# Performance work log

Hardware: AMD Instinct MI355X
Metric: run time of the kernel (lower is better)

The kernel has to match this reference:

```python
import jax, jax.numpy as jnp
import numpy as np

B, C, E, H = 2, 2048, 1024, 16
HD = E // H


def setup_inputs() -> dict:
    key = jax.random.key(0)
    k_x, k_len, k_w1, k_b1, k_w2, k_b2 = jax.random.split(key, 6)
    x = jax.random.normal(k_x, (B, C, E), dtype=jnp.float32)
    # pad_mask: True where token is valid; random valid lengths in [C//2, C]
    lengths = jax.random.randint(k_len, (B,), C // 2, C + 1)
    pad_mask = jnp.arange(C)[None, :] < lengths[:, None]  # [B, C] bool
    s1 = 1.0 / np.sqrt(E)
    w_qkv = jax.random.uniform(k_w1, (3 * E, E), jnp.float32, -s1, s1)  # torch Linear weight [out,in]
    b_qkv = jax.random.uniform(k_b1, (3 * E,), jnp.float32, -s1, s1)
    w_out = jax.random.uniform(k_w2, (E, E), jnp.float32, -s1, s1)
    b_out = jax.random.uniform(k_b2, (E,), jnp.float32, -s1, s1)
    return {"x": x, "pad_mask": pad_mask, "w_qkv": w_qkv, "b_qkv": b_qkv,
            "w_out": w_out, "b_out": b_out}


def reference(x, pad_mask, w_qkv, b_qkv, w_out, b_out):
    b, c, e = x.shape
    qkv = x @ w_qkv.T + b_qkv                      # [B, C, 3E]
    qkv = qkv.reshape(b, c, 3, H, HD)
    qkv = jnp.transpose(qkv, (2, 0, 3, 1, 4))      # [3, B, H, C, HD]
    q, k, v = qkv[0], qkv[1], qkv[2]
    scores = jnp.einsum('bhqd,bhkd->bhqk', q, k) / np.sqrt(HD)  # [B,H,C,C]
    causal = jnp.tril(jnp.ones((c, c), dtype=bool))
    scores = jnp.where(causal[None, None, :, :], scores, -1e9)
    scores = jnp.where(pad_mask[:, None, None, :], scores, -1e9)
    attn = jax.nn.softmax(scores, axis=-1)
    out = jnp.einsum('bhqk,bhkd->bhqd', attn, v)   # [B,H,C,HD]
    out = jnp.transpose(out, (0, 2, 1, 3)).reshape(b, c, e)
    return out @ w_out.T + b_out
```

## Files before the change

kernel.cpp:

```cpp
#include <hip/hip_runtime.h>
#include <cstdint>
#include <cstddef>

typedef short short8 __attribute__((ext_vector_type(8)));
typedef float f32x4 __attribute__((ext_vector_type(4)));

#define NB 2
#define NC 2048
#define NE 1024
#define NH 16
#define ND 64
#define QSZ (NB*NH*NC*ND)

typedef const __attribute__((address_space(1))) void GV;
typedef __attribute__((address_space(3))) void LV;

__device__ __forceinline__ unsigned short f32_to_bf16(float f) {
    union { float f; unsigned u; } v; v.f = f;
    return (unsigned short)((v.u + 0x7fffu + ((v.u >> 16) & 1u)) >> 16);
}

__global__ __launch_bounds__(256) void fused_cast_kernel(
    const float* __restrict__ x, const float* __restrict__ wqkv,
    const float* __restrict__ wout, const void* __restrict__ pad,
    unsigned short* __restrict__ x_bf, unsigned short* __restrict__ wqkv_bf,
    unsigned short* __restrict__ wout_bf, int* __restrict__ lengths)
{
    const int bid = blockIdx.x, tid = threadIdx.x;
    if (bid < 8192) {
        const float* src; unsigned short* dst; int i;
        if (bid < 4096)      { src = x;    dst = x_bf;    i = bid*256 + tid; }
        else if (bid < 7168) { src = wqkv; dst = wqkv_bf; i = (bid-4096)*256 + tid; }
        else                 { src = wout; dst = wout_bf; i = (bid-7168)*256 + tid; }
        float4 v = ((const float4*)src)[i];
        ushort4 o;
        o.x = f32_to_bf16(v.x); o.y = f32_to_bf16(v.y);
        o.z = f32_to_bf16(v.z); o.w = f32_to_bf16(v.w);
        ((ushort4*)dst)[i] = o;
    } else {
        const int b = bid - 8192;
        unsigned w0 = ((const unsigned*)pad)[0];
        int cnt = 0;
        for (int i = tid; i < NC; i += 256) {
            int idx = b*NC + i;
            bool valid;
            if (w0 == 1u)               valid = ((const int*)pad)[idx] != 0;
            else if (w0 == 0x3f800000u) valid = ((const float*)pad)[idx] != 0.0f;
            else                        valid = ((const unsigned char*)pad)[idx] != 0;
            cnt += valid ? 1 : 0;
        }
        cnt += __shfl_xor(cnt, 1);  cnt += __shfl_xor(cnt, 2);
        cnt += __shfl_xor(cnt, 4);  cnt += __shfl_xor(cnt, 8);
        cnt += __shfl_xor(cnt, 16); cnt += __shfl_xor(cnt, 32);
        __shared__ int ws_[4];
        if ((tid & 63) == 0) ws_[tid >> 6] = cnt;
        __syncthreads();
        if (tid == 0) lengths[b] = ws_[0] + ws_[1] + ws_[2] + ws_[3];
    }
}

template<int EPI, int TM, int WPE>
__global__ __launch_bounds__(256, WPE) void gemm_bt_kernel(
    const unsigned short* __restrict__ A,
    const unsigned short* __restrict__ Bw,
    const float* __restrict__ bias,
    const int* __restrict__ lengths,
    float* __restrict__ outF,
    unsigned short* __restrict__ outQ,
    int M, int N, int K)
{
    constexpr int NF = (TM == 128) ? 4 : 2;
    constexpr int WCW = 16 * NF;
    __shared__ unsigned short As[TM*64];
    __shared__ unsigned short Bs[128*64];
    const int tid = threadIdx.x;
    const int w = tid >> 6, lane = tid & 63;
    const int wr = (TM == 128) ? (w >> 1) : 0;
    const int wc = (TM == 128) ? (w & 1) : w;
    const int g = lane >> 4, lr = lane & 15;
    const int nbx = N >> 7, nwg = gridDim.x;
    const int id = blockIdx.x;
    const int swz = (id & 7) * (nwg >> 3) + (id >> 3);
    const int mBase = (swz / nbx) * TM, nBase = (swz % nbx) * 128;

    if constexpr (EPI == 1) {
        if (nBase >= 1024) {
            const int lb = lengths[mBase >> 11];
            if ((mBase & 2047) >= ((lb + 63) & ~63)) return;
        }
    }

    f32x4 acc[4][NF];
#pragma unroll
    for (int m = 0; m < 4; ++m)
#pragma unroll
        for (int n = 0; n < NF; ++n) acc[m][n] = (f32x4){0.f, 0.f, 0.f, 0.f};

    constexpr int AJ = TM / 32;
    int srow[4], scol[4]; unsigned ldso[4];
#pragma unroll
    for (int j = 0; j < 4; ++j) {
        int o = ((j*4 + w) << 10) + lane*16;
        int row = o >> 7;
        int chunk = ((o >> 4) & 7) ^ (row & 7);
        srow[j] = row; scol[j] = chunk * 8; ldso[j] = (unsigned)((j*4 + w) << 10);
    }

    const int nk = K >> 6;
    for (int kt = 0; kt < nk; ++kt) {
        const int k0 = kt << 6;
#pragma unroll
        for (int j = 0; j < AJ; ++j) {
            const unsigned short* ga = A + (size_t)(mBase + srow[j])*K + (k0 + scol[j]);
            __builtin_amdgcn_global_load_lds((GV*)ga, (LV*)((char*)As + ldso[j]), 16, 0, 0);
        }
#pragma unroll
        for (int j = 0; j < 4; ++j) {
            const unsigned short* gb = Bw + (size_t)(nBase + srow[j])*K + (k0 + scol[j]);
            __builtin_amdgcn_global_load_lds((GV*)gb, (LV*)((char*)Bs + ldso[j]), 16, 0, 0);
        }
        __syncthreads();
#pragma unroll
        for (int ks = 0; ks < 2; ++ks) {
            short8 af[4], bf[NF];
#pragma unroll
            for (int m = 0; m < 4; ++m) {
                int row = wr*64 + m*16 + lr;
                int chunk = (ks*4 + g) ^ (row & 7);
                af[m] = *(const short8*)((const char*)As + row*128 + chunk*16);
            }
#pragma unroll
            for (int n = 0; n < NF; ++n) {
                int row = wc*WCW + n*16 + lr;
                int chunk = (ks*4 + g) ^ (row & 7);
                bf[n] = *(const short8*)((const char*)Bs + row*128 + chunk*16);
            }
#pragma unroll
            for (int m = 0; m < 4; ++m)
#pragma unroll
                for (int n = 0; n < NF; ++n)
                    acc[m][n] = __builtin_amdgcn_mfma_f32_16x16x32_bf16(af[m], bf[n], acc[m][n], 0, 0, 0);
        }
        __syncthreads();
    }

    if constexpr (EPI == 0) {
#pragma unroll
        for (int n = 0; n < NF; ++n) {
            int col = nBase + wc*WCW + n*16 + lr;
            float bv = bias[col];
#pragma unroll
            for (int m = 0; m < 4; ++m) {
                int rowb = mBase + wr*64 + m*16 + 4*g;
#pragma unroll
                for (int r = 0; r < 4; ++r)
                    outF[(size_t)(rowb + r)*N + col] = acc[m][n][r] + bv;
            }
        }
    } else {
        if (nBase >= 2048) {
#pragma unroll
            for (int n = 0; n < NF; ++n) {
                int col = nBase + wc*WCW + n*16 + lr;
                float bv = bias[col];
                int hh = (col >> 6) & 15, d = col & 63;
#pragma unroll
                for (int m = 0; m < 4; ++m) {
                    int rowb = mBase + wr*64 + m*16 + 4*g;
                    int bb = rowb >> 11, c = rowb & 2047;
                    int cp = (c & ~63) | ((m >> 1) << 5) | (g << 3) | ((m & 1) << 2);
                    size_t base = (((size_t)((4 + bb)*16 + hh))*64 + d)*2048 + cp;
                    float v0 = acc[m][n][0] + bv, v1 = acc[m][n][1] + bv;
                    float v2 = acc[m][n][2] + bv, v3 = acc[m][n][3] + bv;
                    unsigned w0, w1;
                    asm("v_cvt_pk_bf16_f32 %0, %1, %2" : "=v"(w0) : "v"(v0), "v"(v1));
                    asm("v_cvt_pk_bf16_f32 %0, %1, %2" : "=v"(w1) : "v"(v2), "v"(v3));
                    union { unsigned u[2]; uint2 v; } pk2; pk2.u[0] = w0; pk2.u[1] = w1;
                    *(uint2*)(outQ + base) = pk2.v;
                }
            }
        } else {
#pragma unroll
            for (int n = 0; n < NF; ++n) {
                int col = nBase + wc*WCW + n*16 + lr;
                float bv = bias[col];
                int t = col >> 10, hh = (col >> 6) & 15, d = col & 63;
                float qscale = (t == 0) ? 0.1803368801f : 1.0f;
#pragma unroll
                for (int m = 0; m < 4; ++m) {
                    int rowb = mBase + wr*64 + m*16 + 4*g;
#pragma unroll
                    for (int r = 0; r < 4; ++r) {
                        int row = rowb + r;
                        int bb = row >> 11, c = row & 2047;
                        unsigned short bf16v = f32_to_bf16((acc[m][n][r] + bv) * qscale);
                        size_t idx = ((((size_t)(t*2 + bb))*16 + hh)*2048 + c)*64 + d;
                        outQ[idx] = bf16v;
                    }
                }
            }
        }
    }
}

__global__ __launch_bounds__(256, 4) void attn_kernel(
    const unsigned short* __restrict__ qkv,
    const int* __restrict__ lengths,
    unsigned short* __restrict__ ctx)
{
    __shared__ unsigned short KVt[4][64*64];
    const int bh = blockIdx.x;
    const int b = bh >> 4, h = bh & 15;
    const int y = blockIdx.y;
    const int qb = (y < 8) ? 31 - y : (y < 16) ? y - 8 : (y < 24) ? 39 - y : y - 16;
    const int q0 = qb * 64;
    const int len = lengths[b];
    const int nt = min(qb + 1, (len + 63) >> 6);
    const int tid = threadIdx.x, w = tid >> 6, lane = tid & 63;
    const int g = lane >> 4, lr = lane & 15;
    const unsigned short* qp = qkv +          ((size_t)(b*NH + h))*NC*ND;
    const unsigned short* kp = qkv + QSZ    + ((size_t)(b*NH + h))*NC*ND;
    const unsigned short* vp = qkv + 2*QSZ  + ((size_t)(b*NH + h))*ND*NC;
    const int qw0 = q0 + w*16;

    short8 aq[2];
#pragma unroll
    for (int ks = 0; ks < 2; ++ks)
        aq[ks] = *(const short8*)(qp + (size_t)(qw0 + lr)*ND + ks*32 + 8*g);

    f32x4 oa[4];
#pragma unroll
    for (int n = 0; n < 4; ++n) oa[n] = (f32x4){0.f, 0.f, 0.f, 0.f};
    f32x4 acc_l = (f32x4){0.f, 0.f, 0.f, 0.f};
    union { unsigned u[4]; short8 s; } ones;
    ones.u[0] = ones.u[1] = ones.u[2] = ones.u[3] = 0x3F803F80u;

    const char* kv0 = (char*)KVt + lr*128 + (((g    ) ^ (lr & 7)) << 4);
    const char* kv1 = (char*)KVt + lr*128 + (((4 + g) ^ (lr & 7)) << 4);

    int srw0, sck0, srw1, sck1; unsigned ldso0, ldso1;
    {
        int o0 = (w << 10) + lane*16;
        int r0 = o0 >> 7;
        sck0 = (((o0 >> 4) & 7) ^ (r0 & 7)) * 8; srw0 = r0;
        ldso0 = (unsigned)(w << 10);
        int o1 = ((4 + w) << 10) + lane*16;
        int r1 = o1 >> 7;
        sck1 = (((o1 >> 4) & 7) ^ (r1 & 7)) * 8; srw1 = r1;
        ldso1 = (unsigned)((4 + w) << 10);
    }
    const unsigned short* gk0 = kp + (size_t)srw0*ND + sck0;
    const unsigned short* gk1 = kp + (size_t)srw1*ND + sck1;
    const unsigned short* gv0 = vp + (size_t)srw0*NC + sck0;
    const unsigned short* gv1 = vp + (size_t)srw1*NC + sck1;

#define STAGE(BUF) do {                                                           \
    __builtin_amdgcn_global_load_lds((GV*)gk0, (LV*)((char*)KVt + (BUF)*8192 + ldso0), 16, 0, 0);          \
    __builtin_amdgcn_global_load_lds((GV*)gv0, (LV*)((char*)KVt + 16384 + (BUF)*8192 + ldso0), 16, 0, 0);  \
    __builtin_amdgcn_global_load_lds((GV*)gk1, (LV*)((char*)KVt + (BUF)*8192 + ldso1), 16, 0, 0);          \
    __builtin_amdgcn_global_load_lds((GV*)gv1, (LV*)((char*)KVt + 16384 + (BUF)*8192 + ldso1), 16, 0, 0);  \
    gk0 += 64*ND; gk1 += 64*ND; gv0 += 64; gv1 += 64; } while (0)

    STAGE(0);
    __syncthreads();

#pragma unroll 2
    for (int t = 0; t < nt - 1; ++t) {
        STAGE((t + 1) & 1);
        const int buf = t & 1;

        f32x4 sa[4];
#pragma unroll
        for (int a = 0; a < 4; ++a) sa[a] = (f32x4){0.f, 0.f, 0.f, 0.f};
        __builtin_amdgcn_s_setprio(1);
#pragma unroll
        for (int a = 0; a < 4; ++a) {
            short8 ak = *(const short8*)(kv0 + buf*8192 + a*2048);
            sa[a] = __builtin_amdgcn_mfma_f32_16x16x32_bf16(ak, aq[0], sa[a], 0, 0, 0);
        }
#pragma unroll
        for (int a = 0; a < 4; ++a) {
            short8 ak = *(const short8*)(kv1 + buf*8192 + a*2048);
            sa[a] = __builtin_amdgcn_mfma_f32_16x16x32_bf16(ak, aq[1], sa[a], 0, 0, 0);
        }
        __builtin_amdgcn_s_setprio(0);

        float p[4][4];
#pragma unroll
        for (int a = 0; a < 4; ++a)
#pragma unroll
            for (int r = 0; r < 4; ++r)
                p[a][r] = __builtin_amdgcn_exp2f(sa[a][r]);

        unsigned pw0, pw1, pw2, pw3, pw4, pw5, pw6, pw7;
        asm("v_cvt_pk_bf16_f32 %0, %1, %2" : "=v"(pw0) : "v"(p[0][0]), "v"(p[0][1]));
        asm("v_cvt_pk_bf16_f32 %0, %1, %2" : "=v"(pw1) : "v"(p[0][2]), "v"(p[0][3]));
        asm("v_cvt_pk_bf16_f32 %0, %1, %2" : "=v"(pw2) : "v"(p[1][0]), "v"(p[1][1]));
        asm("v_cvt_pk_bf16_f32 %0, %1, %2" : "=v"(pw3) : "v"(p[1][2]), "v"(p[1][3]));
        asm("v_cvt_pk_bf16_f32 %0, %1, %2" : "=v"(pw4) : "v"(p[2][0]), "v"(p[2][1]));
        asm("v_cvt_pk_bf16_f32 %0, %1, %2" : "=v"(pw5) : "v"(p[2][2]), "v"(p[2][3]));
        asm("v_cvt_pk_bf16_f32 %0, %1, %2" : "=v"(pw6) : "v"(p[3][0]), "v"(p[3][1]));
        asm("v_cvt_pk_bf16_f32 %0, %1, %2" : "=v"(pw7) : "v"(p[3][2]), "v"(p[3][3]));
        union { unsigned u[4]; short8 s; } pu0, pu1;
        pu0.u[0] = pw0; pu0.u[1] = pw1; pu0.u[2] = pw2; pu0.u[3] = pw3;
        pu1.u[0] = pw4; pu1.u[1] = pw5; pu1.u[2] = pw6; pu1.u[3] = pw7;

        __builtin_amdgcn_s_setprio(1);
        acc_l = __builtin_amdgcn_mfma_f32_16x16x32_bf16(pu0.s, ones.s, acc_l, 0, 0, 0);
#pragma unroll
        for (int n = 0; n < 4; ++n) {
            short8 bv = *(const short8*)(kv0 + 16384 + buf*8192 + n*2048);
            oa[n] = __builtin_amdgcn_mfma_f32_16x16x32_bf16(pu0.s, bv, oa[n], 0, 0, 0);
        }
        acc_l = __builtin_amdgcn_mfma_f32_16x16x32_bf16(pu1.s, ones.s, acc_l, 0, 0, 0);
#pragma unroll
        for (int n = 0; n < 4; ++n) {
            short8 bv = *(const short8*)(kv1 + 16384 + buf*8192 + n*2048);
            oa[n] = __builtin_amdgcn_mfma_f32_16x16x32_bf16(pu1.s, bv, oa[n], 0, 0, 0);
        }
        __builtin_amdgcn_s_setprio(0);

        __syncthreads();
    }

    {
        const int t = nt - 1;
        const int boff = (t & 1) * 8192;
        const char* k0b = kv0 + boff;
        const char* k1b = kv1 + boff;
        const int thr = min(qw0 + lr, len - 1);
        const int kb0 = (t << 6) + 4*g;

        f32x4 sa[4];
#pragma unroll
        for (int a = 0; a < 4; ++a) sa[a] = (f32x4){0.f, 0.f, 0.f, 0.f};
        __builtin_amdgcn_s_setprio(1);
#pragma unroll
        for (int a = 0; a < 4; ++a) {
            short8 ak = *(const short8*)(k0b + a*2048);
            sa[a] = __builtin_amdgcn_mfma_f32_16x16x32_bf16(ak, aq[0], sa[a], 0, 0, 0);
        }
#pragma unroll
        for (int a = 0; a < 4; ++a) {
            short8 ak = *(const short8*)(k1b + a*2048);
            sa[a] = __builtin_amdgcn_mfma_f32_16x16x32_bf16(ak, aq[1], sa[a], 0, 0, 0);
        }
        __builtin_amdgcn_s_setprio(0);

        float p[4][4];
#pragma unroll
        for (int a = 0; a < 4; ++a)
#pragma unroll
            for (int r = 0; r < 4; ++r) {
                int key = kb0 + 16*a + r;
                p[a][r] = (key <= thr) ? __builtin_amdgcn_exp2f(sa[a][r]) : 0.f;
            }

        unsigned pw0, pw1, pw2, pw3, pw4, pw5, pw6, pw7;
        asm("v_cvt_pk_bf16_f32 %0, %1, %2" : "=v"(pw0) : "v"(p[0][0]), "v"(p[0][1]));
        asm("v_cvt_pk_bf16_f32 %0, %1, %2" : "=v"(pw1) : "v"(p[0][2]), "v"(p[0][3]));
        asm("v_cvt_pk_bf16_f32 %0, %1, %2" : "=v"(pw2) : "v"(p[1][0]), "v"(p[1][1]));
        asm("v_cvt_pk_bf16_f32 %0, %1, %2" : "=v"(pw3) : "v"(p[1][2]), "v"(p[1][3]));
        asm("v_cvt_pk_bf16_f32 %0, %1, %2" : "=v"(pw4) : "v"(p[2][0]), "v"(p[2][1]));
        asm("v_cvt_pk_bf16_f32 %0, %1, %2" : "=v"(pw5) : "v"(p[2][2]), "v"(p[2][3]));
        asm("v_cvt_pk_bf16_f32 %0, %1, %2" : "=v"(pw6) : "v"(p[3][0]), "v"(p[3][1]));
        asm("v_cvt_pk_bf16_f32 %0, %1, %2" : "=v"(pw7) : "v"(p[3][2]), "v"(p[3][3]));
        union { unsigned u[4]; short8 s; } pu0, pu1;
        pu0.u[0] = pw0; pu0.u[1] = pw1; pu0.u[2] = pw2; pu0.u[3] = pw3;
        pu1.u[0] = pw4; pu1.u[1] = pw5; pu1.u[2] = pw6; pu1.u[3] = pw7;

        __builtin_amdgcn_s_setprio(1);
        acc_l = __builtin_amdgcn_mfma_f32_16x16x32_bf16(pu0.s, ones.s, acc_l, 0, 0, 0);
#pragma unroll
        for (int n = 0; n < 4; ++n) {
            short8 bv = *(const short8*)(k0b + 16384 + n*2048);
            oa[n] = __builtin_amdgcn_mfma_f32_16x16x32_bf16(pu0.s, bv, oa[n], 0, 0, 0);
        }
        acc_l = __builtin_amdgcn_mfma_f32_16x16x32_bf16(pu1.s, ones.s, acc_l, 0, 0, 0);
#pragma unroll
        for (int n = 0; n < 4; ++n) {
            short8 bv = *(const short8*)(k1b + 16384 + n*2048);
            oa[n] = __builtin_amdgcn_mfma_f32_16x16x32_bf16(pu1.s, bv, oa[n], 0, 0, 0);
        }
        __builtin_amdgcn_s_setprio(0);
    }
#undef STAGE

#pragma unroll
    for (int r = 0; r < 4; ++r) {
        float inv = __builtin_amdgcn_rcpf(acc_l[r]);
        int qg = qw0 + 4*g + r;
        size_t base = ((size_t)b*NC + qg)*NE + h*ND;
#pragma unroll
        for (int n = 0; n < 4; ++n)
            ctx[base + n*16 + lr] = f32_to_bf16(oa[n][r] * inv);
    }
}

extern "C" void kernel_launch(void* const* d_in, const int* in_sizes, int n_in,
                              void* d_out, int out_size, void* d_ws, size_t ws_size,
                              hipStream_t stream)
{
    const float* x    = (const float*)d_in[0];
    const void*  pad  = d_in[1];
    const float* wqkv = (const float*)d_in[2];
    const float* bqkv = (const float*)d_in[3];
    const float* wout = (const float*)d_in[4];
    const float* bout = (const float*)d_in[5];
    float* out = (float*)d_out;

    unsigned short* x_bf    = (unsigned short*)d_ws;
    unsigned short* wqkv_bf = x_bf    + 4194304;
    unsigned short* wout_bf = wqkv_bf + 3145728;
    unsigned short* qkv     = wout_bf + 1048576;
    unsigned short* ctx     = qkv     + 12582912;
    int*            lens    = (int*)(ctx + 4194304);

    fused_cast_kernel<<<8194, 256, 0, stream>>>(x, wqkv, wout, pad,
                                                x_bf, wqkv_bf, wout_bf, lens);

    gemm_bt_kernel<1,128,3><<<768, 256, 0, stream>>>(x_bf, wqkv_bf, bqkv, lens,
                                                     nullptr, qkv, 4096, 3072, 1024);
    attn_kernel<<<dim3(32, 32), 256, 0, stream>>>(qkv, lens, ctx);
    gemm_bt_kernel<0,64,2><<<512, 256, 0, stream>>>(ctx, wout_bf, bout, lens,
                                                    out, nullptr, 4096, 1024, 1024);
}
```

Before: 83.65 us.

## Split long causal attention query blocks across two KV halves with merge kernel

Query blocks 16-31 now process their keys in two launches: keys 0-1023 in one block and keys 1024 onward in another. Both write unnormalized partial outputs and row sums in fp32 to workspace, and a new merge kernel adds them, normalizes and writes bf16 context. This splits the long causal rows so the per-block work is more even and more blocks run in parallel. The cost is an extra kernel launch and fp32 partial traffic through global memory. Merging without a running max is safe only because the existing kernel already uses plain exp2 with no max subtraction.

```diff
diff --git a/kernel.cpp b/kernel.cpp
--- a/kernel.cpp
+++ b/kernel.cpp
@@ -206,16 +206,22 @@
 __global__ __launch_bounds__(256, 4) void attn_kernel(
     const unsigned short* __restrict__ qkv,
     const int* __restrict__ lengths,
-    unsigned short* __restrict__ ctx)
+    unsigned short* __restrict__ ctx,
+    float* __restrict__ paO,
+    float* __restrict__ paL)
 {
     __shared__ unsigned short KVt[4][64*64];
     const int bh = blockIdx.x;
     const int b = bh >> 4, h = bh & 15;
     const int y = blockIdx.y;
-    const int qb = (y < 8) ? 31 - y : (y < 16) ? y - 8 : (y < 24) ? 39 - y : y - 16;
+    int qb, c0, mode;
+    if (y < 16)      { mode = 1; qb = 16 + y;        c0 = 0;  }
+    else if (y < 32) { mode = 0; qb = 31 - y;        c0 = 0;  }
+    else             { mode = 2; qb = 16 + (47 - y); c0 = 16; }
     const int q0 = qb * 64;
     const int len = lengths[b];
-    const int nt = min(qb + 1, (len + 63) >> 6);
+    const int lenceil = (len + 63) >> 6;
+    const int c1 = (mode == 1) ? 16 : min(qb + 1, lenceil);
     const int tid = threadIdx.x, w = tid >> 6, lane = tid & 63;
     const int g = lane >> 4, lr = lane & 15;
     const unsigned short* qp = qkv +          ((size_t)(b*NH + h))*NC*ND;
@@ -249,10 +255,10 @@
         sck1 = (((o1 >> 4) & 7) ^ (r1 & 7)) * 8; srw1 = r1;
         ldso1 = (unsigned)((4 + w) << 10);
     }
-    const unsigned short* gk0 = kp + (size_t)srw0*ND + sck0;
-    const unsigned short* gk1 = kp + (size_t)srw1*ND + sck1;
-    const unsigned short* gv0 = vp + (size_t)srw0*NC + sck0;
-    const unsigned short* gv1 = vp + (size_t)srw1*NC + sck1;
+    const unsigned short* gk0 = kp + (size_t)(c0*64 + srw0)*ND + sck0;
+    const unsigned short* gk1 = kp + (size_t)(c0*64 + srw1)*ND + sck1;
+    const unsigned short* gv0 = vp + (size_t)srw0*NC + c0*64 + sck0;
+    const unsigned short* gv1 = vp + (size_t)srw1*NC + c0*64 + sck1;
 
 #define STAGE(BUF) do {                                                           \
     __builtin_amdgcn_global_load_lds((GV*)gk0, (LV*)((char*)KVt + (BUF)*8192 + ldso0), 16, 0, 0);          \
@@ -261,139 +267,178 @@
     __builtin_amdgcn_global_load_lds((GV*)gv1, (LV*)((char*)KVt + 16384 + (BUF)*8192 + ldso1), 16, 0, 0);  \
     gk0 += 64*ND; gk1 += 64*ND; gv0 += 64; gv1 += 64; } while (0)
 
-    STAGE(0);
-    __syncthreads();
-
+    if (!(mode == 2 && c1 <= 16)) {
+        STAGE(0);
+        __syncthreads();
+
+        const int nfast = ((mode == 1) ? c1 : c1 - 1) - c0;
 #pragma unroll 2
-    for (int t = 0; t < nt - 1; ++t) {
-        STAGE((t + 1) & 1);
-        const int buf = t & 1;
-
-        f32x4 sa[4];
-#pragma unroll
-        for (int a = 0; a < 4; ++a) sa[a] = (f32x4){0.f, 0.f, 0.f, 0.f};
-        __builtin_amdgcn_s_setprio(1);
-#pragma unroll
-        for (int a = 0; a < 4; ++a) {
-            short8 ak = *(const short8*)(kv0 + buf*8192 + a*2048);
-            sa[a] = __builtin_amdgcn_mfma_f32_16x16x32_bf16(ak, aq[0], sa[a], 0, 0, 0);
-        }
-#pragma unroll
-        for (int a = 0; a < 4; ++a) {
-            short8 ak = *(const short8*)(kv1 + buf*8192 + a*2048);
-            sa[a] = __builtin_amdgcn_mfma_f32_16x16x32_bf16(ak, aq[1], sa[a], 0, 0, 0);
-        }
-        __builtin_amdgcn_s_setprio(0);
-
-        float p[4][4];
-#pragma unroll
-        for (int a = 0; a < 4; ++a)
-#pragma unroll
-            for (int r = 0; r < 4; ++r)
-                p[a][r] = __builtin_amdgcn_exp2f(sa[a][r]);
-
-        unsigned pw0, pw1, pw2, pw3, pw4, pw5, pw6, pw7;
-        asm("v_cvt_pk_bf16_f32 %0, %1, %2" : "=v"(pw0) : "v"(p[0][0]), "v"(p[0][1]));
-        asm("v_cvt_pk_bf16_f32 %0, %1, %2" : "=v"(pw1) : "v"(p[0][2]), "v"(p[0][3]));
-        asm("v_cvt_pk_bf16_f32 %0, %1, %2" : "=v"(pw2) : "v"(p[1][0]), "v"(p[1][1]));
-        asm("v_cvt_pk_bf16_f32 %0, %1, %2" : "=v"(pw3) : "v"(p[1][2]), "v"(p[1][3]));
-        asm("v_cvt_pk_bf16_f32 %0, %1, %2" : "=v"(pw4) : "v"(p[2][0]), "v"(p[2][1]));
-        asm("v_cvt_pk_bf16_f32 %0, %1, %2" : "=v"(pw5) : "v"(p[2][2]), "v"(p[2][3]));
-        asm("v_cvt_pk_bf16_f32 %0, %1, %2" : "=v"(pw6) : "v"(p[3][0]), "v"(p[3][1]));
-        asm("v_cvt_pk_bf16_f32 %0, %1, %2" : "=v"(pw7) : "v"(p[3][2]), "v"(p[3][3]));
-        union { unsigned u[4]; short8 s; } pu0, pu1;
-        pu0.u[0] = pw0; pu0.u[1] = pw1; pu0.u[2] = pw2; pu0.u[3] = pw3;
-        pu1.u[0] = pw4; pu1.u[1] = pw5; pu1.u[2] = pw6; pu1.u[3] = pw7;
-
-        __builtin_amdgcn_s_setprio(1);
-        acc_l = __builtin_amdgcn_mfma_f32_16x16x32_bf16(pu0.s, ones.s, acc_l, 0, 0, 0);
-#pragma unroll
-        for (int n = 0; n < 4; ++n) {
-            short8 bv = *(const short8*)(kv0 + 16384 + buf*8192 + n*2048);
-            oa[n] = __builtin_amdgcn_mfma_f32_16x16x32_bf16(pu0.s, bv, oa[n], 0, 0, 0);
-        }
-        acc_l = __builtin_amdgcn_mfma_f32_16x16x32_bf16(pu1.s, ones.s, acc_l, 0, 0, 0);
-#pragma unroll
-        for (int n = 0; n < 4; ++n) {
-            short8 bv = *(const short8*)(kv1 + 16384 + buf*8192 + n*2048);
-            oa[n] = __builtin_amdgcn_mfma_f32_16x16x32_bf16(pu1.s, bv, oa[n], 0, 0, 0);
-        }
-        __builtin_amdgcn_s_setprio(0);
-
-        __syncthreads();
-    }
-
-    {
-        const int t = nt - 1;
-        const int boff = (t & 1) * 8192;
-        const char* k0b = kv0 + boff;
-        const char* k1b = kv1 + boff;
-        const int thr = min(qw0 + lr, len - 1);
-        const int kb0 = (t << 6) + 4*g;
-
-        f32x4 sa[4];
-#pragma unroll
-        for (int a = 0; a < 4; ++a) sa[a] = (f32x4){0.f, 0.f, 0.f, 0.f};
-        __builtin_amdgcn_s_setprio(1);
-#pragma unroll
-        for (int a = 0; a < 4; ++a) {
-            short8 ak = *(const short8*)(k0b + a*2048);
-            sa[a] = __builtin_amdgcn_mfma_f32_16x16x32_bf16(ak, aq[0], sa[a], 0, 0, 0);
-        }
-#pragma unroll
-        for (int a = 0; a < 4; ++a) {
-            short8 ak = *(const short8*)(k1b + a*2048);
-            sa[a] = __builtin_amdgcn_mfma_f32_16x16x32_bf16(ak, aq[1], sa[a], 0, 0, 0);
-        }
-        __builtin_amdgcn_s_setprio(0);
-
-        float p[4][4];
-#pragma unroll
-        for (int a = 0; a < 4; ++a)
-#pragma unroll
-            for (int r = 0; r < 4; ++r) {
-                int key = kb0 + 16*a + r;
-                p[a][r] = (key <= thr) ? __builtin_amdgcn_exp2f(sa[a][r]) : 0.f;
-            }
-
-        unsigned pw0, pw1, pw2, pw3, pw4, pw5, pw6, pw7;
-        asm("v_cvt_pk_bf16_f32 %0, %1, %2" : "=v"(pw0) : "v"(p[0][0]), "v"(p[0][1]));
-        asm("v_cvt_pk_bf16_f32 %0, %1, %2" : "=v"(pw1) : "v"(p[0][2]), "v"(p[0][3]));
-        asm("v_cvt_pk_bf16_f32 %0, %1, %2" : "=v"(pw2) : "v"(p[1][0]), "v"(p[1][1]));
-        asm("v_cvt_pk_bf16_f32 %0, %1, %2" : "=v"(pw3) : "v"(p[1][2]), "v"(p[1][3]));
-        asm("v_cvt_pk_bf16_f32 %0, %1, %2" : "=v"(pw4) : "v"(p[2][0]), "v"(p[2][1]));
-        asm("v_cvt_pk_bf16_f32 %0, %1, %2" : "=v"(pw5) : "v"(p[2][2]), "v"(p[2][3]));
-        asm("v_cvt_pk_bf16_f32 %0, %1, %2" : "=v"(pw6) : "v"(p[3][0]), "v"(p[3][1]));
-        asm("v_cvt_pk_bf16_f32 %0, %1, %2" : "=v"(pw7) : "v"(p[3][2]), "v"(p[3][3]));
-        union { unsigned u[4]; short8 s; } pu0, pu1;
-        pu0.u[0] = pw0; pu0.u[1] = pw1; pu0.u[2] = pw2; pu0.u[3] = pw3;
-        pu1.u[0] = pw4; pu1.u[1] = pw5; pu1.u[2] = pw6; pu1.u[3] = pw7;
-
-        __builtin_amdgcn_s_setprio(1);
-        acc_l = __builtin_amdgcn_mfma_f32_16x16x32_bf16(pu0.s, ones.s, acc_l, 0, 0, 0);
-#pragma unroll
-        for (int n = 0; n < 4; ++n) {
-            short8 bv = *(const short8*)(k0b + 16384 + n*2048);
-            oa[n] = __builtin_amdgcn_mfma_f32_16x16x32_bf16(pu0.s, bv, oa[n], 0, 0, 0);
-        }
-        acc_l = __builtin_amdgcn_mfma_f32_16x16x32_bf16(pu1.s, ones.s, acc_l, 0, 0, 0);
-#pragma unroll
-        for (int n = 0; n < 4; ++n) {
-            short8 bv = *(const short8*)(k1b + 16384 + n*2048);
-            oa[n] = __builtin_amdgcn_mfma_f32_16x16x32_bf16(pu1.s, bv, oa[n], 0, 0, 0);
-        }
-        __builtin_amdgcn_s_setprio(0);
+        for (int tt = 0; tt < nfast; ++tt) {
+            STAGE((tt + 1) & 1);
+            const int buf = tt & 1;
+
+            f32x4 sa[4];
+#pragma unroll
+            for (int a = 0; a < 4; ++a) sa[a] = (f32x4){0.f, 0.f, 0.f, 0.f};
+            __builtin_amdgcn_s_setprio(1);
+#pragma unroll
+            for (int a = 0; a < 4; ++a) {
+                short8 ak = *(const short8*)(kv0 + buf*8192 + a*2048);
+                sa[a] = __builtin_amdgcn_mfma_f32_16x16x32_bf16(ak, aq[0], sa[a], 0, 0, 0);
+            }
+#pragma unroll
+            for (int a = 0; a < 4; ++a) {
+                short8 ak = *(const short8*)(kv1 + buf*8192 + a*2048);
+                sa[a] = __builtin_amdgcn_mfma_f32_16x16x32_bf16(ak, aq[1], sa[a], 0, 0, 0);
+            }
+            __builtin_amdgcn_s_setprio(0);
+
+            float p[4][4];
+#pragma unroll
+            for (int a = 0; a < 4; ++a)
+#pragma unroll
+                for (int r = 0; r < 4; ++r)
+                    p[a][r] = __builtin_amdgcn_exp2f(sa[a][r]);
+
+            unsigned pw0, pw1, pw2, pw3, pw4, pw5, pw6, pw7;
+            asm("v_cvt_pk_bf16_f32 %0, %1, %2" : "=v"(pw0) : "v"(p[0][0]), "v"(p[0][1]));
+            asm("v_cvt_pk_bf16_f32 %0, %1, %2" : "=v"(pw1) : "v"(p[0][2]), "v"(p[0][3]));
+            asm("v_cvt_pk_bf16_f32 %0, %1, %2" : "=v"(pw2) : "v"(p[1][0]), "v"(p[1][1]));
+            asm("v_cvt_pk_bf16_f32 %0, %1, %2" : "=v"(pw3) : "v"(p[1][2]), "v"(p[1][3]));
+            asm("v_cvt_pk_bf16_f32 %0, %1, %2" : "=v"(pw4) : "v"(p[2][0]), "v"(p[2][1]));
+            asm("v_cvt_pk_bf16_f32 %0, %1, %2" : "=v"(pw5) : "v"(p[2][2]), "v"(p[2][3]));
+            asm("v_cvt_pk_bf16_f32 %0, %1, %2" : "=v"(pw6) : "v"(p[3][0]), "v"(p[3][1]));
+            asm("v_cvt_pk_bf16_f32 %0, %1, %2" : "=v"(pw7) : "v"(p[3][2]), "v"(p[3][3]));
+            union { unsigned u[4]; short8 s; } pu0, pu1;
+            pu0.u[0] = pw0; pu0.u[1] = pw1; pu0.u[2] = pw2; pu0.u[3] = pw3;
+            pu1.u[0] = pw4; pu1.u[1] = pw5; pu1.u[2] = pw6; pu1.u[3] = pw7;
+
+            __builtin_amdgcn_s_setprio(1);
+            acc_l = __builtin_amdgcn_mfma_f32_16x16x32_bf16(pu0.s, ones.s, acc_l, 0, 0, 0);
+#pragma unroll
+            for (int n = 0; n < 4; ++n) {
+                short8 bv = *(const short8*)(kv0 + 16384 + buf*8192 + n*2048);
+                oa[n] = __builtin_amdgcn_mfma_f32_16x16x32_bf16(pu0.s, bv, oa[n], 0, 0, 0);
+            }
+            acc_l = __builtin_amdgcn_mfma_f32_16x16x32_bf16(pu1.s, ones.s, acc_l, 0, 0, 0);
+#pragma unroll
+            for (int n = 0; n < 4; ++n) {
+                short8 bv = *(const short8*)(kv1 + 16384 + buf*8192 + n*2048);
+                oa[n] = __builtin_amdgcn_mfma_f32_16x16x32_bf16(pu1.s, bv, oa[n], 0, 0, 0);
+            }
+            __builtin_amdgcn_s_setprio(0);
+
+            __syncthreads();
+        }
+
+        if (mode != 1) {
+            const int boff = (nfast & 1) * 8192;
+            const char* k0b = kv0 + boff;
+            const char* k1b = kv1 + boff;
+            const int thr = min(qw0 + lr, len - 1);
+            const int kb0 = ((c1 - 1) << 6) + 4*g;
+
+            f32x4 sa[4];
+#pragma unroll
+            for (int a = 0; a < 4; ++a) sa[a] = (f32x4){0.f, 0.f, 0.f, 0.f};
+            __builtin_amdgcn_s_setprio(1);
+#pragma unroll
+            for (int a = 0; a < 4; ++a) {
+                short8 ak = *(const short8*)(k0b + a*2048);
+                sa[a] = __builtin_amdgcn_mfma_f32_16x16x32_bf16(ak, aq[0], sa[a], 0, 0, 0);
+            }
+#pragma unroll
+            for (int a = 0; a < 4; ++a) {
+                short8 ak = *(const short8*)(k1b + a*2048);
+                sa[a] = __builtin_amdgcn_mfma_f32_16x16x32_bf16(ak, aq[1], sa[a], 0, 0, 0);
+            }
+            __builtin_amdgcn_s_setprio(0);
+
+            float p[4][4];
+#pragma unroll
+            for (int a = 0; a < 4; ++a)
+#pragma unroll
+                for (int r = 0; r < 4; ++r) {
+                    int key = kb0 + 16*a + r;
+                    p[a][r] = (key <= thr) ? __builtin_amdgcn_exp2f(sa[a][r]) : 0.f;
+                }
+
+            unsigned pw0, pw1, pw2, pw3, pw4, pw5, pw6, pw7;
+            asm("v_cvt_pk_bf16_f32 %0, %1, %2" : "=v"(pw0) : "v"(p[0][0]), "v"(p[0][1]));
+            asm("v_cvt_pk_bf16_f32 %0, %1, %2" : "=v"(pw1) : "v"(p[0][2]), "v"(p[0][3]));
+            asm("v_cvt_pk_bf16_f32 %0, %1, %2" : "=v"(pw2) : "v"(p[1][0]), "v"(p[1][1]));
+            asm("v_cvt_pk_bf16_f32 %0, %1, %2" : "=v"(pw3) : "v"(p[1][2]), "v"(p[1][3]));
+            asm("v_cvt_pk_bf16_f32 %0, %1, %2" : "=v"(pw4) : "v"(p[2][0]), "v"(p[2][1]));
+            asm("v_cvt_pk_bf16_f32 %0, %1, %2" : "=v"(pw5) : "v"(p[2][2]), "v"(p[2][3]));
+            asm("v_cvt_pk_bf16_f32 %0, %1, %2" : "=v"(pw6) : "v"(p[3][0]), "v"(p[3][1]));
+            asm("v_cvt_pk_bf16_f32 %0, %1, %2" : "=v"(pw7) : "v"(p[3][2]), "v"(p[3][3]));
+            union { unsigned u[4]; short8 s; } pu0, pu1;
+            pu0.u[0] = pw0; pu0.u[1] = pw1; pu0.u[2] = pw2; pu0.u[3] = pw3;
+            pu1.u[0] = pw4; pu1.u[1] = pw5; pu1.u[2] = pw6; pu1.u[3] = pw7;
+
+            __builtin_amdgcn_s_setprio(1);
+            acc_l = __builtin_amdgcn_mfma_f32_16x16x32_bf16(pu0.s, ones.s, acc_l, 0, 0, 0);
+#pragma unroll
+            for (int n = 0; n < 4; ++n) {
+                short8 bv = *(const short8*)(k0b + 16384 + n*2048);
+                oa[n] = __builtin_amdgcn_mfma_f32_16x16x32_bf16(pu0.s, bv, oa[n], 0, 0, 0);
+            }
+            acc_l = __builtin_amdgcn_mfma_f32_16x16x32_bf16(pu1.s, ones.s, acc_l, 0, 0, 0);
+#pragma unroll
+            for (int n = 0; n < 4; ++n) {
+                short8 bv = *(const short8*)(k1b + 16384 + n*2048);
+                oa[n] = __builtin_amdgcn_mfma_f32_16x16x32_bf16(pu1.s, bv, oa[n], 0, 0, 0);
+            }
+            __builtin_amdgcn_s_setprio(0);
+        }
     }
 #undef STAGE
 
-#pragma unroll
-    for (int r = 0; r < 4; ++r) {
-        float inv = __builtin_amdgcn_rcpf(acc_l[r]);
-        int qg = qw0 + 4*g + r;
-        size_t base = ((size_t)b*NC + qg)*NE + h*ND;
-#pragma unroll
-        for (int n = 0; n < 4; ++n)
-            ctx[base + n*16 + lr] = f32_to_bf16(oa[n][r] * inv);
+    if (mode == 0) {
+#pragma unroll
+        for (int r = 0; r < 4; ++r) {
+            float inv = __builtin_amdgcn_rcpf(acc_l[r]);
+            int qg = qw0 + 4*g + r;
+            size_t base = ((size_t)b*NC + qg)*NE + h*ND;
+#pragma unroll
+            for (int n = 0; n < 4; ++n)
+                ctx[base + n*16 + lr] = f32_to_bf16(oa[n][r] * inv);
+        }
+    } else {
+        const int grp = bh*16 + (qb - 16);
+        float* po = paO + (size_t)(mode - 1)*2097152 + (size_t)grp*4096;
+        float* pl = paL + (mode - 1)*32768 + grp*64;
+#pragma unroll
+        for (int r = 0; r < 4; ++r) {
+            int prow = w*16 + 4*g + r;
+            pl[prow] = acc_l[r];
+#pragma unroll
+            for (int n = 0; n < 4; ++n)
+                po[prow*64 + n*16 + lr] = oa[n][r];
+        }
+    }
+}
+
+__global__ __launch_bounds__(256) void attn_merge_kernel(
+    const float* __restrict__ paO, const float* __restrict__ paL,
+    unsigned short* __restrict__ ctx)
+{
+    const int grp = blockIdx.x;
+    const int bh = grp >> 4, qm = grp & 15;
+    const int b = bh >> 4, h = bh & 15;
+    const int qb = 16 + qm;
+    const float* oA = paO + (size_t)grp*4096;
+    const float* oB = oA + 2097152;
+    const float* lA = paL + grp*64;
+    const float* lB = lA + 32768;
+#pragma unroll
+    for (int i = 0; i < 16; ++i) {
+        int idx = threadIdx.x + i*256;
+        int row = idx >> 6, d = idx & 63;
+        float l = lA[row] + lB[row];
+        float v = (oA[idx] + oB[idx]) * __builtin_amdgcn_rcpf(l);
+        int qg = qb*64 + row;
+        ctx[((size_t)(b*NC + qg))*NE + h*ND + d] = f32_to_bf16(v);
     }
 }
 
@@ -415,13 +460,16 @@
     unsigned short* qkv     = wout_bf + 1048576;
     unsigned short* ctx     = qkv     + 12582912;
     int*            lens    = (int*)(ctx + 4194304);
+    float*          paO     = (float*)((char*)d_ws + 50331712);
+    float*          paL     = paO + 2*2097152;
 
     fused_cast_kernel<<<8194, 256, 0, stream>>>(x, wqkv, wout, pad,
                                                 x_bf, wqkv_bf, wout_bf, lens);
 
     gemm_bt_kernel<1,128,3><<<768, 256, 0, stream>>>(x_bf, wqkv_bf, bqkv, lens,
                                                      nullptr, qkv, 4096, 3072, 1024);
-    attn_kernel<<<dim3(32, 32), 256, 0, stream>>>(qkv, lens, ctx);
+    attn_kernel<<<dim3(32, 48), 256, 0, stream>>>(qkv, lens, ctx, paO, paL);
+    attn_merge_kernel<<<512, 256, 0, stream>>>(paO, paL, ctx);
     gemm_bt_kernel<0,64,2><<<512, 256, 0, stream>>>(ctx, wout_bf, bout, lens,
                                                     out, nullptr, 4096, 1024, 1024);
 }
```

Result: slower. 89.80 us (+7.4%).

## Triple-buffer K/V tiles in attention with one barrier per iteration

Applied to the files above, without the earlier changes.

The attention kernel's shared K/V staging moves from double to triple buffering. Two tiles are prefetched up front. Each iteration waits with a partial `s_waitcnt vmcnt(4)` plus a raw barrier, instead of a full `__syncthreads` at the end of the loop. This keeps two tile loads in flight while the current tile is computed, hiding more global-load latency. In exchange, shared memory rises from 32 KB to 48 KB per block, and launch bounds drop to 3 blocks per CU, which reduces occupancy. The prefetch also reads one tile past the causal range, which may read slightly out of bounds at the end of the buffer.

```diff
diff --git a/kernel.cpp b/kernel.cpp
--- a/kernel.cpp
+++ b/kernel.cpp
@@ -203,12 +203,12 @@
     }
 }
 
-__global__ __launch_bounds__(256, 4) void attn_kernel(
+__global__ __launch_bounds__(256, 3) void attn_kernel(
     const unsigned short* __restrict__ qkv,
     const int* __restrict__ lengths,
     unsigned short* __restrict__ ctx)
 {
-    __shared__ unsigned short KVt[4][64*64];
+    __shared__ unsigned short KVt[6][64*64];
     const int bh = blockIdx.x;
     const int b = bh >> 4, h = bh & 15;
     const int y = blockIdx.y;
@@ -255,19 +255,26 @@
     const unsigned short* gv1 = vp + (size_t)srw1*NC + sck1;
 
 #define STAGE(BUF) do {                                                           \
-    __builtin_amdgcn_global_load_lds((GV*)gk0, (LV*)((char*)KVt + (BUF)*8192 + ldso0), 16, 0, 0);          \
-    __builtin_amdgcn_global_load_lds((GV*)gv0, (LV*)((char*)KVt + 16384 + (BUF)*8192 + ldso0), 16, 0, 0);  \
-    __builtin_amdgcn_global_load_lds((GV*)gk1, (LV*)((char*)KVt + (BUF)*8192 + ldso1), 16, 0, 0);          \
-    __builtin_amdgcn_global_load_lds((GV*)gv1, (LV*)((char*)KVt + 16384 + (BUF)*8192 + ldso1), 16, 0, 0);  \
+    __builtin_amdgcn_global_load_lds((GV*)gk0, (LV*)((char*)KVt + (unsigned)(BUF)*8192u + ldso0), 16, 0, 0);          \
+    __builtin_amdgcn_global_load_lds((GV*)gv0, (LV*)((char*)KVt + 24576u + (unsigned)(BUF)*8192u + ldso0), 16, 0, 0); \
+    __builtin_amdgcn_global_load_lds((GV*)gk1, (LV*)((char*)KVt + (unsigned)(BUF)*8192u + ldso1), 16, 0, 0);          \
+    __builtin_amdgcn_global_load_lds((GV*)gv1, (LV*)((char*)KVt + 24576u + (unsigned)(BUF)*8192u + ldso1), 16, 0, 0); \
     gk0 += 64*ND; gk1 += 64*ND; gv0 += 64; gv1 += 64; } while (0)
 
     STAGE(0);
-    __syncthreads();
-
-#pragma unroll 2
-    for (int t = 0; t < nt - 1; ++t) {
-        STAGE((t + 1) & 1);
-        const int buf = t & 1;
+    STAGE(1);
+
+    int rbuf = 0, sbuf = 2;
+    const int nfast = nt - 1;
+    for (int t = 0; t < nfast; ++t) {
+        asm volatile("s_waitcnt vmcnt(4)" ::: "memory");
+        __builtin_amdgcn_s_barrier();
+        STAGE(sbuf);
+        sbuf = (sbuf == 2) ? 0 : sbuf + 1;
+        const int ko = rbuf * 8192;
+        rbuf = (rbuf == 2) ? 0 : rbuf + 1;
+        const char* kA = kv0 + ko;
+        const char* kB = kv1 + ko;
 
         f32x4 sa[4];
 #pragma unroll
@@ -275,12 +282,12 @@
         __builtin_amdgcn_s_setprio(1);
 #pragma unroll
         for (int a = 0; a < 4; ++a) {
-            short8 ak = *(const short8*)(kv0 + buf*8192 + a*2048);
+            short8 ak = *(const short8*)(kA + a*2048);
             sa[a] = __builtin_amdgcn_mfma_f32_16x16x32_bf16(ak, aq[0], sa[a], 0, 0, 0);
         }
 #pragma unroll
         for (int a = 0; a < 4; ++a) {
-            short8 ak = *(const short8*)(kv1 + buf*8192 + a*2048);
+            short8 ak = *(const short8*)(kB + a*2048);
             sa[a] = __builtin_amdgcn_mfma_f32_16x16x32_bf16(ak, aq[1], sa[a], 0, 0, 0);
         }
         __builtin_amdgcn_s_setprio(0);
@@ -309,27 +316,25 @@
         acc_l = __builtin_amdgcn_mfma_f32_16x16x32_bf16(pu0.s, ones.s, acc_l, 0, 0, 0);
 #pragma unroll
         for (int n = 0; n < 4; ++n) {
-            short8 bv = *(const short8*)(kv0 + 16384 + buf*8192 + n*2048);
+            short8 bv = *(const short8*)(kA + 24576 + n*2048);
             oa[n] = __builtin_amdgcn_mfma_f32_16x16x32_bf16(pu0.s, bv, oa[n], 0, 0, 0);
         }
         acc_l = __builtin_amdgcn_mfma_f32_16x16x32_bf16(pu1.s, ones.s, acc_l, 0, 0, 0);
 #pragma unroll
         for (int n = 0; n < 4; ++n) {
-            short8 bv = *(const short8*)(kv1 + 16384 + buf*8192 + n*2048);
+            short8 bv = *(const short8*)(kB + 24576 + n*2048);
             oa[n] = __builtin_amdgcn_mfma_f32_16x16x32_bf16(pu1.s, bv, oa[n], 0, 0, 0);
         }
         __builtin_amdgcn_s_setprio(0);
-
+    }
+
+    {
         __syncthreads();
-    }
-
-    {
-        const int t = nt - 1;
-        const int boff = (t & 1) * 8192;
-        const char* k0b = kv0 + boff;
-        const char* k1b = kv1 + boff;
+        const int ko = rbuf * 8192;
+        const char* kA = kv0 + ko;
+        const char* kB = kv1 + ko;
         const int thr = min(qw0 + lr, len - 1);
-        const int kb0 = (t << 6) + 4*g;
+        const int kb0 = ((nt - 1) << 6) + 4*g;
 
         f32x4 sa[4];
 #pragma unroll
@@ -337,12 +342,12 @@
         __builtin_amdgcn_s_setprio(1);
 #pragma unroll
         for (int a = 0; a < 4; ++a) {
-            short8 ak = *(const short8*)(k0b + a*2048);
+            short8 ak = *(const short8*)(kA + a*2048);
             sa[a] = __builtin_amdgcn_mfma_f32_16x16x32_bf16(ak, aq[0], sa[a], 0, 0, 0);
         }
 #pragma unroll
         for (int a = 0; a < 4; ++a) {
-            short8 ak = *(const short8*)(k1b + a*2048);
+            short8 ak = *(const short8*)(kB + a*2048);
             sa[a] = __builtin_amdgcn_mfma_f32_16x16x32_bf16(ak, aq[1], sa[a], 0, 0, 0);
         }
         __builtin_amdgcn_s_setprio(0);
@@ -373,13 +378,13 @@
         acc_l = __builtin_amdgcn_mfma_f32_16x16x32_bf16(pu0.s, ones.s, acc_l, 0, 0, 0);
 #pragma unroll
         for (int n = 0; n < 4; ++n) {
-            short8 bv = *(const short8*)(k0b + 16384 + n*2048);
+            short8 bv = *(const short8*)(kA + 24576 + n*2048);
             oa[n] = __builtin_amdgcn_mfma_f32_16x16x32_bf16(pu0.s, bv, oa[n], 0, 0, 0);
         }
         acc_l = __builtin_amdgcn_mfma_f32_16x16x32_bf16(pu1.s, ones.s, acc_l, 0, 0, 0);
 #pragma unroll
         for (int n = 0; n < 4; ++n) {
-            short8 bv = *(const short8*)(k1b + 16384 + n*2048);
+            short8 bv = *(const short8*)(kB + 24576 + n*2048);
             oa[n] = __builtin_amdgcn_mfma_f32_16x16x32_bf16(pu1.s, bv, oa[n], 0, 0, 0);
         }
         __builtin_amdgcn_s_setprio(0);
```

Result: no change. 84.65 us (+1.2%).
